# Optimization experiments

Measured on AMD Instinct MI355X. Metric: run time of the kernel, lower is better.

Reference implementation:

```python
import jax, jax.numpy as jnp
import numpy as np

N = 50000      # nodes
E = 800000     # edges
G = 64         # graphs in batch
H = 256        # hidden_channels
CE = 128       # coord embed dim = H//2
OTH = 6        # in_channels - 3
ED = 8         # edge_dim
EE = 128       # edge_embedding_dim
GD = 16        # global_dim
L = 3          # num_layers


def setup_inputs() -> dict:
    key = jax.random.key(0)
    ks = jax.random.split(key, 24)
    s = 0.05
    inp = {
        "x": jax.random.normal(ks[0], (N, 9), jnp.float32),
        "edge_index": jax.random.randint(ks[1], (2, E), 0, N),
        "batch": jnp.sort(jax.random.randint(ks[2], (N,), 0, G)),
        "edge_attr": jax.random.normal(ks[3], (E, ED), jnp.float32),
        "global_x": jax.random.normal(ks[4], (G, GD), jnp.float32),
        # coordinate embedder (Linear 3->128 + relu)
        "coord_W": jax.random.normal(ks[5], (3, CE), jnp.float32) * s,
        "coord_b": jnp.zeros((CE,), jnp.float32),
        # node_mlp (Linear 6->128 + relu)
        "node_W": jax.random.normal(ks[6], (OTH, CE), jnp.float32) * s,
        "node_b": jnp.zeros((CE,), jnp.float32),
        # edge processor (Linear 8->128 + relu) and projection 128->256
        "edge_W": jax.random.normal(ks[7], (ED, EE), jnp.float32) * s,
        "edge_b": jnp.zeros((EE,), jnp.float32),
        "proj_W": jax.random.normal(ks[8], (EE, H), jnp.float32) * s,
        "proj_b": jnp.zeros((H,), jnp.float32),
        # stacked GCN layer weights
        "gcn_W": jax.random.normal(ks[9], (L, H, H), jnp.float32) * s,
        "gcn_b": jnp.zeros((L, H), jnp.float32),
        # attention pooling
        "attn_w": jax.random.normal(ks[10], (H,), jnp.float32) * s,
        "attn_b": jnp.zeros((), jnp.float32),
        # global_mlp: Linear 16->256, relu, Linear 256->256
        "gmlp_W1": jax.random.normal(ks[11], (GD, H), jnp.float32) * s,
        "gmlp_b1": jnp.zeros((H,), jnp.float32),
        "gmlp_W2": jax.random.normal(ks[12], (H, H), jnp.float32) * s,
        "gmlp_b2": jnp.zeros((H,), jnp.float32),
        # fc_out: Linear 512->256, relu, Linear 256->1
        "fc_W1": jax.random.normal(ks[13], (2 * H, H), jnp.float32) * s,
        "fc_b1": jnp.zeros((H,), jnp.float32),
        "fc_W2": jax.random.normal(ks[14], (H, 1), jnp.float32) * s,
        "fc_b2": jnp.zeros((1,), jnp.float32),
    }
    return inp


def _segsum(v, idx, num):
    return jax.ops.segment_sum(v, idx, num_segments=num)


def reference(x, edge_index, batch, edge_attr, global_x,
              coord_W, coord_b, node_W, node_b, edge_W, edge_b,
              proj_W, proj_b, gcn_W, gcn_b, attn_w, attn_b,
              gmlp_W1, gmlp_b1, gmlp_W2, gmlp_b2,
              fc_W1, fc_b1, fc_W2, fc_b2):
    relu = jax.nn.relu
    # --- node embedding: coords + other features ---
    coord_emb = relu(x[:, :3] @ coord_W + coord_b)          # [N, 128]
    other_emb = relu(x[:, 3:] @ node_W + node_b)            # [N, 128]
    x_emb = jnp.concatenate([coord_emb, other_emb], axis=1)  # [N, 256]

    # --- edge embedding, aggregated to target nodes (index_add over col) ---
    edge_emb = relu(edge_attr @ edge_W + edge_b) @ proj_W + proj_b  # [E, 256]
    col0 = edge_index[1]
    node_msg = _segsum(edge_emb, col0, N)                    # [N, 256]

    # --- GCN normalization with self-loops ---
    sl = jnp.arange(N)
    row = jnp.concatenate([edge_index[0], sl])
    col = jnp.concatenate([edge_index[1], sl])
    deg = _segsum(jnp.ones_like(col, jnp.float32), col, N)   # >= 1
    dnorm = jax.lax.rsqrt(deg)
    efac = (dnorm[row] * dnorm[col])[:, None]                # [E+N, 1]

    # --- stacked GCN layers (edge messages re-added each layer, per source) ---
    for i in range(L):
        x_in = x_emb + node_msg
        h = x_in @ gcn_W[i]                                  # [N, 256]
        x_emb = _segsum(h[row] * efac, col, N) + gcn_b[i]
        if i < L - 1:
            x_emb = relu(x_emb)

    # --- attention pooling (per-graph softmax over batch index) ---
    scores = x_emb @ attn_w + attn_b                         # [N]
    m = jax.ops.segment_max(scores, batch, num_segments=G)
    e = jnp.exp(scores - m[batch])
    denom = _segsum(e, batch, G)
    attn = e / denom[batch]
    graph_emb = _segsum(x_emb * attn[:, None], batch, G)     # [G, 256]

    # --- global features + head ---
    g = relu(global_x @ gmlp_W1 + gmlp_b1) @ gmlp_W2 + gmlp_b2
    hcat = jnp.concatenate([graph_emb, g], axis=-1)          # [G, 512]
    out = relu(hcat @ fc_W1 + fc_b1) @ fc_W2 + fc_b2         # [G, 1]
    return out
```

## Files before the change

kernel.cpp:

```cpp
#include <hip/hip_runtime.h>


typedef float f32x4 __attribute__((ext_vector_type(4)));
typedef short s16x8 __attribute__((ext_vector_type(8)));

__device__ __forceinline__ unsigned short f2bf(float f) {
  union { float f; unsigned u; } v{f};
  unsigned r = v.u + 0x7fff + ((v.u >> 16) & 1);
  return (unsigned short)(r >> 16);
}
__device__ __forceinline__ float bf2f(unsigned short s) {
  union { unsigned u; float f; } v{(unsigned)s << 16};
  return v.f;
}
__device__ __forceinline__ float blo(unsigned u) {
  union { unsigned x; float f; } v{u << 16};
  return v.f;
}
__device__ __forceinline__ float bhi(unsigned u) {
  union { unsigned x; float f; } v{u & 0xffff0000u};
  return v.f;
}
__device__ __forceinline__ unsigned pk2(float a, float b) {
  return (unsigned)f2bf(a) | ((unsigned)f2bf(b) << 16);
}

__global__ void node_embed_kernel(const float* __restrict__ x,
                                  const float* __restrict__ coord_W, const float* __restrict__ coord_b,
                                  const float* __restrict__ node_W, const float* __restrict__ node_b,
                                  short* __restrict__ x0, int N) {
  int tid = threadIdx.x;
  int node = blockIdx.x * 8 + (tid >> 5);
  if (node >= N) return;
  int ch0 = (tid & 31) * 8;
  const float* xr = x + (size_t)node * 9;
  float a[8];
  if (ch0 < 128) {
    float4 b0 = *(const float4*)&coord_b[ch0];
    float4 b1 = *(const float4*)&coord_b[ch0 + 4];
    a[0]=b0.x; a[1]=b0.y; a[2]=b0.z; a[3]=b0.w; a[4]=b1.x; a[5]=b1.y; a[6]=b1.z; a[7]=b1.w;
#pragma unroll
    for (int k = 0; k < 3; k++) {
      float xv = xr[k];
      float4 w0 = *(const float4*)&coord_W[k * 128 + ch0];
      float4 w1 = *(const float4*)&coord_W[k * 128 + ch0 + 4];
      a[0] = fmaf(xv, w0.x, a[0]); a[1] = fmaf(xv, w0.y, a[1]);
      a[2] = fmaf(xv, w0.z, a[2]); a[3] = fmaf(xv, w0.w, a[3]);
      a[4] = fmaf(xv, w1.x, a[4]); a[5] = fmaf(xv, w1.y, a[5]);
      a[6] = fmaf(xv, w1.z, a[6]); a[7] = fmaf(xv, w1.w, a[7]);
    }
  } else {
    int c0 = ch0 - 128;
    float4 b0 = *(const float4*)&node_b[c0];
    float4 b1 = *(const float4*)&node_b[c0 + 4];
    a[0]=b0.x; a[1]=b0.y; a[2]=b0.z; a[3]=b0.w; a[4]=b1.x; a[5]=b1.y; a[6]=b1.z; a[7]=b1.w;
#pragma unroll
    for (int k = 0; k < 6; k++) {
      float xv = xr[3 + k];
      float4 w0 = *(const float4*)&node_W[k * 128 + c0];
      float4 w1 = *(const float4*)&node_W[k * 128 + c0 + 4];
      a[0] = fmaf(xv, w0.x, a[0]); a[1] = fmaf(xv, w0.y, a[1]);
      a[2] = fmaf(xv, w0.z, a[2]); a[3] = fmaf(xv, w0.w, a[3]);
      a[4] = fmaf(xv, w1.x, a[4]); a[5] = fmaf(xv, w1.y, a[5]);
      a[6] = fmaf(xv, w1.z, a[6]); a[7] = fmaf(xv, w1.w, a[7]);
    }
  }
  uint4 o;
  o.x = pk2(fmaxf(a[0], 0.f), fmaxf(a[1], 0.f));
  o.y = pk2(fmaxf(a[2], 0.f), fmaxf(a[3], 0.f));
  o.z = pk2(fmaxf(a[4], 0.f), fmaxf(a[5], 0.f));
  o.w = pk2(fmaxf(a[6], 0.f), fmaxf(a[7], 0.f));
  *(uint4*)&x0[(size_t)node * 256 + ch0] = o;
}

__global__ void count_kernel(const int* __restrict__ col, int* __restrict__ cnt, int E) {
  int e = blockIdx.x * 256 + threadIdx.x;
  if (e < E) atomicAdd(&cnt[col[e]], 1);
}

__global__ void breduce_kernel(const int* __restrict__ cnt, int* __restrict__ partials, int N) {
  __shared__ int red[256];
  int t = threadIdx.x;
  int i = blockIdx.x * 256 + t;
  int v = (i < N) ? cnt[i] : 0;
  red[t] = v;
  __syncthreads();
  for (int off = 128; off; off >>= 1) {
    if (t < off) red[t] += red[t + off];
    __syncthreads();
  }
  if (t == 0) partials[blockIdx.x] = red[0];
}

__global__ void scan_partials_kernel(int* __restrict__ partials, int nb) {
  __shared__ int s[1024];
  int t = threadIdx.x;
  for (int i = t; i < nb; i += 256) s[i] = partials[i];
  __syncthreads();
  if (t == 0) {
    int run = 0;
    for (int i = 0; i < nb; i++) { int c = s[i]; s[i] = run; run += c; }
  }
  __syncthreads();
  for (int i = t; i < nb; i += 256) partials[i] = s[i];
}

__global__ void scan_apply_kernel(const int* __restrict__ cnt, const int* __restrict__ partials,
                                  int* __restrict__ rowstart, float* __restrict__ dnorm,
                                  int* __restrict__ cursor, int N) {
  __shared__ int red[256];
  int t = threadIdx.x;
  int i = blockIdx.x * 256 + t;
  int v = (i < N) ? cnt[i] : 0;
  red[t] = v;
  __syncthreads();
  for (int off = 1; off < 256; off <<= 1) {
    int x = (t >= off) ? red[t - off] : 0;
    __syncthreads();
    red[t] += x;
    __syncthreads();
  }
  if (i < N) {
    int ex = red[t] - v + partials[blockIdx.x];
    rowstart[i] = ex;
    dnorm[i] = rsqrtf((float)(v + 1));
    cursor[i] = 0;
    if (i == N - 1) rowstart[N] = ex + v;
  }
}

__global__ void scatter_kernel(const int* __restrict__ row, const int* __restrict__ col,
                               const int* __restrict__ rowstart, int* __restrict__ cursor,
                               const float* __restrict__ dnorm,
                               int2* __restrict__ pk8, int* __restrict__ eids, int E) {
  int e = blockIdx.x * 256 + threadIdx.x;
  if (e >= E) return;
  int c = col[e], r = row[e];
  int p = atomicAdd(&cursor[c], 1);
  int slot = rowstart[c] + p;
  pk8[slot] = make_int2(r, __float_as_int(dnorm[r] * dnorm[c]));
  eids[slot] = e;
}

__global__ void wt_kernel(const float* __restrict__ gcn_W, const float* __restrict__ proj_W,
                          short* __restrict__ gcnWt, short* __restrict__ projWt) {
  int idx = blockIdx.x * 256 + threadIdx.x;
  if (idx < 3 * 65536) {
    int l = idx >> 16, r = idx & 65535, n = r >> 8, k = r & 255;
    gcnWt[idx] = (short)f2bf(gcn_W[l * 65536 + k * 256 + n]);
  } else {
    int j = idx - 3 * 65536;
    int n = j >> 7, k = j & 127;
    projWt[j] = (short)f2bf(proj_W[k * 256 + n]);
  }
}

__global__ void __launch_bounds__(256) edge_msg_kernel(
    const float* __restrict__ edge_attr, const int* __restrict__ eids,
    const int* __restrict__ rowstart,
    const float* __restrict__ edge_W, const float* __restrict__ edge_b,
    unsigned* __restrict__ msg128u, int N) {
  int lane = threadIdx.x & 63;
  int node = blockIdx.x * 4 + (threadIdx.x >> 6);
  if (node >= N) return;
  int ch0 = lane * 2;
  float wa[8], wb[8];
#pragma unroll
  for (int k = 0; k < 8; k++) {
    float2 w = *(const float2*)&edge_W[k * 128 + ch0];
    wa[k] = w.x; wb[k] = w.y;
  }
  float2 bb = *(const float2*)&edge_b[ch0];
  float acc0 = 0.f, acc1 = 0.f;
  int s = rowstart[node], s1 = rowstart[node + 1];
  const float4* ea4 = (const float4*)edge_attr;
  for (; s + 4 <= s1; s += 4) {
    int e0 = eids[s], e1 = eids[s + 1], e2 = eids[s + 2], e3 = eids[s + 3];
    float4 a00 = ea4[(size_t)e0 * 2], a01 = ea4[(size_t)e0 * 2 + 1];
    float4 a10 = ea4[(size_t)e1 * 2], a11 = ea4[(size_t)e1 * 2 + 1];
    float4 a20 = ea4[(size_t)e2 * 2], a21 = ea4[(size_t)e2 * 2 + 1];
    float4 a30 = ea4[(size_t)e3 * 2], a31 = ea4[(size_t)e3 * 2 + 1];
    float t0, t1;
#define EMLP(lo, hi)                                                        \
    t0 = bb.x; t1 = bb.y;                                                   \
    t0 = fmaf(lo.x, wa[0], t0); t1 = fmaf(lo.x, wb[0], t1);                 \
    t0 = fmaf(lo.y, wa[1], t0); t1 = fmaf(lo.y, wb[1], t1);                 \
    t0 = fmaf(lo.z, wa[2], t0); t1 = fmaf(lo.z, wb[2], t1);                 \
    t0 = fmaf(lo.w, wa[3], t0); t1 = fmaf(lo.w, wb[3], t1);                 \
    t0 = fmaf(hi.x, wa[4], t0); t1 = fmaf(hi.x, wb[4], t1);                 \
    t0 = fmaf(hi.y, wa[5], t0); t1 = fmaf(hi.y, wb[5], t1);                 \
    t0 = fmaf(hi.z, wa[6], t0); t1 = fmaf(hi.z, wb[6], t1);                 \
    t0 = fmaf(hi.w, wa[7], t0); t1 = fmaf(hi.w, wb[7], t1);                 \
    acc0 += fmaxf(t0, 0.f); acc1 += fmaxf(t1, 0.f);
    EMLP(a00, a01)
    EMLP(a10, a11)
    EMLP(a20, a21)
    EMLP(a30, a31)
  }
  for (; s < s1; s++) {
    int e = eids[s];
    float4 lo = ea4[(size_t)e * 2], hi = ea4[(size_t)e * 2 + 1];
    float t0, t1;
    EMLP(lo, hi)
  }
#undef EMLP
  msg128u[(size_t)node * 64 + lane] = pk2(acc0, acc1);
}

__global__ void __launch_bounds__(256) proj_gemm_mfma(
    const short* __restrict__ msg128, const short* __restrict__ projWt,
    const float* __restrict__ proj_b, const int* __restrict__ cnt,
    short* __restrict__ node_msg, int N) {
  __shared__ short As[64][136];
  int tid = threadIdx.x;
  int n0 = blockIdx.x * 64;
  for (int i = tid; i < 64 * 32; i += 256) {
    int r = i >> 5, c4 = (i & 31) << 2;
    int n = n0 + r;
    uint2 v = make_uint2(0, 0);
    if (n < N) v = *(const uint2*)&msg128[(size_t)n * 128 + c4];
    *(uint2*)&As[r][c4] = v;
  }
  __syncthreads();
  int wave = tid >> 6, lane = tid & 63;
  int mrow = wave * 16 + (lane & 15);
  int kgrp = (lane >> 4) * 8;
  f32x4 acc[16];
#pragma unroll
  for (int i = 0; i < 16; i++) acc[i] = (f32x4){0.f, 0.f, 0.f, 0.f};
  const short* wbase = projWt + (size_t)(lane & 15) * 128 + kgrp;
#pragma unroll
  for (int kk = 0; kk < 4; kk++) {
    s16x8 a = *(const s16x8*)&As[mrow][kk * 32 + kgrp];
#pragma unroll
    for (int nf = 0; nf < 16; nf++) {
      s16x8 b = *(const s16x8*)&wbase[(size_t)nf * 16 * 128 + kk * 32];
      acc[nf] = __builtin_amdgcn_mfma_f32_16x16x32_bf16(a, b, acc[nf], 0, 0, 0);
    }
  }
  int orow0 = wave * 16 + (lane >> 4) * 4;
  int ocol = lane & 15;
#pragma unroll
  for (int r = 0; r < 4; r++) {
    int n = n0 + orow0 + r;
    if (n < N) {
      float cn = (float)cnt[n];
#pragma unroll
      for (int nf = 0; nf < 16; nf++) {
        int c = nf * 16 + ocol;
        node_msg[(size_t)n * 256 + c] = (short)f2bf(acc[nf][r] + cn * proj_b[c]);
      }
    }
  }
}

__global__ void __launch_bounds__(256) gcn_gemm_add_mfma(
    const short* __restrict__ X, const short* __restrict__ M,
    const short* __restrict__ Wt, short* __restrict__ Hout, int N) {
  __shared__ short As[64][264];
  int tid = threadIdx.x;
  int n0 = blockIdx.x * 64;
  for (int i = tid; i < 64 * 64; i += 256) {
    int r = i >> 6, c4 = (i & 63) << 2;
    int n = n0 + r;
    uint2 o = make_uint2(0, 0);
    if (n < N) {
      uint2 xv = *(const uint2*)&X[(size_t)n * 256 + c4];
      uint2 mv = *(const uint2*)&M[(size_t)n * 256 + c4];
      o.x = pk2(blo(xv.x) + blo(mv.x), bhi(xv.x) + bhi(mv.x));
      o.y = pk2(blo(xv.y) + blo(mv.y), bhi(xv.y) + bhi(mv.y));
    }
    *(uint2*)&As[r][c4] = o;
  }
  __syncthreads();
  int wave = tid >> 6, lane = tid & 63;
  int mrow = wave * 16 + (lane & 15);
  int kgrp = (lane >> 4) * 8;
  f32x4 acc[16];
#pragma unroll
  for (int i = 0; i < 16; i++) acc[i] = (f32x4){0.f, 0.f, 0.f, 0.f};
  const short* wbase = Wt + (size_t)(lane & 15) * 256 + kgrp;
#pragma unroll
  for (int kk = 0; kk < 8; kk++) {
    s16x8 a = *(const s16x8*)&As[mrow][kk * 32 + kgrp];
#pragma unroll
    for (int nf = 0; nf < 16; nf++) {
      s16x8 b = *(const s16x8*)&wbase[(size_t)nf * 16 * 256 + kk * 32];
      acc[nf] = __builtin_amdgcn_mfma_f32_16x16x32_bf16(a, b, acc[nf], 0, 0, 0);
    }
  }
  int orow0 = wave * 16 + (lane >> 4) * 4;
  int ocol = lane & 15;
#pragma unroll
  for (int nf = 0; nf < 16; nf++) {
#pragma unroll
    for (int r = 0; r < 4; r++) {
      int n = n0 + orow0 + r;
      if (n < N) Hout[(size_t)n * 256 + nf * 16 + ocol] = (short)f2bf(acc[nf][r]);
    }
  }
}

__global__ void __launch_bounds__(256) gcn_agg_kernel(
    const short* __restrict__ h, const int2* __restrict__ pk8,
    const int* __restrict__ rowstart, const float* __restrict__ dnorm,
    const float* __restrict__ b, const short* __restrict__ node_msg,
    short* __restrict__ xin, int N) {
  int lane = threadIdx.x & 63;
  int node = blockIdx.x * 4 + (threadIdx.x >> 6);
  if (node >= N) return;
  int ch0 = lane << 2;
  size_t rowb = (size_t)node * 256 + ch0;
  float dn = dnorm[node];
  float wgt = dn * dn;
  uint2 hv = *(const uint2*)&h[rowb];
  float a0 = blo(hv.x) * wgt, a1 = bhi(hv.x) * wgt;
  float a2 = blo(hv.y) * wgt, a3 = bhi(hv.y) * wgt;
  int s = rowstart[node], s1 = rowstart[node + 1];
  for (; s + 4 <= s1; s += 4) {
    int2 p0 = pk8[s], p1 = pk8[s + 1], p2 = pk8[s + 2], p3 = pk8[s + 3];
    float f0 = __int_as_float(p0.y), f1 = __int_as_float(p1.y);
    float f2 = __int_as_float(p2.y), f3 = __int_as_float(p3.y);
    uint2 v0 = *(const uint2*)&h[(size_t)p0.x * 256 + ch0];
    uint2 v1 = *(const uint2*)&h[(size_t)p1.x * 256 + ch0];
    uint2 v2 = *(const uint2*)&h[(size_t)p2.x * 256 + ch0];
    uint2 v3 = *(const uint2*)&h[(size_t)p3.x * 256 + ch0];
    a0 = fmaf(blo(v0.x), f0, a0); a1 = fmaf(bhi(v0.x), f0, a1);
    a2 = fmaf(blo(v0.y), f0, a2); a3 = fmaf(bhi(v0.y), f0, a3);
    a0 = fmaf(blo(v1.x), f1, a0); a1 = fmaf(bhi(v1.x), f1, a1);
    a2 = fmaf(blo(v1.y), f1, a2); a3 = fmaf(bhi(v1.y), f1, a3);
    a0 = fmaf(blo(v2.x), f2, a0); a1 = fmaf(bhi(v2.x), f2, a1);
    a2 = fmaf(blo(v2.y), f2, a2); a3 = fmaf(bhi(v2.y), f2, a3);
    a0 = fmaf(blo(v3.x), f3, a0); a1 = fmaf(bhi(v3.x), f3, a1);
    a2 = fmaf(blo(v3.y), f3, a2); a3 = fmaf(bhi(v3.y), f3, a3);
  }
  for (; s < s1; s++) {
    int2 p = pk8[s];
    float f = __int_as_float(p.y);
    uint2 v = *(const uint2*)&h[(size_t)p.x * 256 + ch0];
    a0 = fmaf(blo(v.x), f, a0); a1 = fmaf(bhi(v.x), f, a1);
    a2 = fmaf(blo(v.y), f, a2); a3 = fmaf(bhi(v.y), f, a3);
  }
  float4 bv = *(const float4*)&b[ch0];
  uint2 mv = *(const uint2*)&node_msg[rowb];
  float y0 = fmaxf(a0 + bv.x, 0.f) + blo(mv.x);
  float y1 = fmaxf(a1 + bv.y, 0.f) + bhi(mv.x);
  float y2 = fmaxf(a2 + bv.z, 0.f) + blo(mv.y);
  float y3 = fmaxf(a3 + bv.w, 0.f) + bhi(mv.y);
  uint2 o;
  o.x = pk2(y0, y1);
  o.y = pk2(y2, y3);
  *(uint2*)&xin[rowb] = o;
}

__global__ void __launch_bounds__(256) gcn_gemm_mfma(
    const short* __restrict__ Xin, const short* __restrict__ Wt,
    short* __restrict__ Hout, int N) {
  __shared__ short As[64][264];
  int tid = threadIdx.x;
  int n0 = blockIdx.x * 64;
  for (int i = tid; i < 64 * 64; i += 256) {
    int r = i >> 6, c4 = (i & 63) << 2;
    int n = n0 + r;
    uint2 v = make_uint2(0, 0);
    if (n < N) v = *(const uint2*)&Xin[(size_t)n * 256 + c4];
    *(uint2*)&As[r][c4] = v;
  }
  __syncthreads();
  int wave = tid >> 6, lane = tid & 63;
  int mrow = wave * 16 + (lane & 15);
  int kgrp = (lane >> 4) * 8;
  f32x4 acc[16];
#pragma unroll
  for (int i = 0; i < 16; i++) acc[i] = (f32x4){0.f, 0.f, 0.f, 0.f};
  const short* wbase = Wt + (size_t)(lane & 15) * 256 + kgrp;
#pragma unroll
  for (int kk = 0; kk < 8; kk++) {
    s16x8 a = *(const s16x8*)&As[mrow][kk * 32 + kgrp];
#pragma unroll
    for (int nf = 0; nf < 16; nf++) {
      s16x8 b = *(const s16x8*)&wbase[(size_t)nf * 16 * 256 + kk * 32];
      acc[nf] = __builtin_amdgcn_mfma_f32_16x16x32_bf16(a, b, acc[nf], 0, 0, 0);
    }
  }
  int orow0 = wave * 16 + (lane >> 4) * 4;
  int ocol = lane & 15;
#pragma unroll
  for (int nf = 0; nf < 16; nf++) {
#pragma unroll
    for (int r = 0; r < 4; r++) {
      int n = n0 + orow0 + r;
      if (n < N) Hout[(size_t)n * 256 + nf * 16 + ocol] = (short)f2bf(acc[nf][r]);
    }
  }
}

__global__ void __launch_bounds__(256) final_agg_kernel(
    const short* __restrict__ h, const int2* __restrict__ pk8,
    const int* __restrict__ rowstart, const float* __restrict__ dnorm,
    const float* __restrict__ b, short* __restrict__ x_emb,
    const float* __restrict__ attn_w, const float* __restrict__ attn_b,
    float* __restrict__ scores, int N) {
  int lane = threadIdx.x & 63;
  int node = blockIdx.x * 4 + (threadIdx.x >> 6);
  if (node >= N) return;
  int ch0 = lane << 2;
  size_t rowb = (size_t)node * 256 + ch0;
  float dn = dnorm[node];
  float wgt = dn * dn;
  uint2 hv = *(const uint2*)&h[rowb];
  float a0 = blo(hv.x) * wgt, a1 = bhi(hv.x) * wgt;
  float a2 = blo(hv.y) * wgt, a3 = bhi(hv.y) * wgt;
  int s = rowstart[node], s1 = rowstart[node + 1];
  for (; s + 4 <= s1; s += 4) {
    int2 p0 = pk8[s], p1 = pk8[s + 1], p2 = pk8[s + 2], p3 = pk8[s + 3];
    float f0 = __int_as_float(p0.y), f1 = __int_as_float(p1.y);
    float f2 = __int_as_float(p2.y), f3 = __int_as_float(p3.y);
    uint2 v0 = *(const uint2*)&h[(size_t)p0.x * 256 + ch0];
    uint2 v1 = *(const uint2*)&h[(size_t)p1.x * 256 + ch0];
    uint2 v2 = *(const uint2*)&h[(size_t)p2.x * 256 + ch0];
    uint2 v3 = *(const uint2*)&h[(size_t)p3.x * 256 + ch0];
    a0 = fmaf(blo(v0.x), f0, a0); a1 = fmaf(bhi(v0.x), f0, a1);
    a2 = fmaf(blo(v0.y), f0, a2); a3 = fmaf(bhi(v0.y), f0, a3);
    a0 = fmaf(blo(v1.x), f1, a0); a1 = fmaf(bhi(v1.x), f1, a1);
    a2 = fmaf(blo(v1.y), f1, a2); a3 = fmaf(bhi(v1.y), f1, a3);
    a0 = fmaf(blo(v2.x), f2, a0); a1 = fmaf(bhi(v2.x), f2, a1);
    a2 = fmaf(blo(v2.y), f2, a2); a3 = fmaf(bhi(v2.y), f2, a3);
    a0 = fmaf(blo(v3.x), f3, a0); a1 = fmaf(bhi(v3.x), f3, a1);
    a2 = fmaf(blo(v3.y), f3, a2); a3 = fmaf(bhi(v3.y), f3, a3);
  }
  for (; s < s1; s++) {
    int2 p = pk8[s];
    float f = __int_as_float(p.y);
    uint2 v = *(const uint2*)&h[(size_t)p.x * 256 + ch0];
    a0 = fmaf(blo(v.x), f, a0); a1 = fmaf(bhi(v.x), f, a1);
    a2 = fmaf(blo(v.y), f, a2); a3 = fmaf(bhi(v.y), f, a3);
  }
  float4 bv = *(const float4*)&b[ch0];
  a0 += bv.x; a1 += bv.y; a2 += bv.z; a3 += bv.w;
  uint2 o;
  o.x = pk2(a0, a1);
  o.y = pk2(a2, a3);
  *(uint2*)&x_emb[rowb] = o;
  float4 aw = *(const float4*)&attn_w[ch0];
  float p = a0 * aw.x + a1 * aw.y + a2 * aw.z + a3 * aw.w;
#pragma unroll
  for (int off = 32; off; off >>= 1) p += __shfl_down(p, off);
  if (lane == 0) scores[node] = p + attn_b[0];
}

__global__ void gse_kernel(const int* __restrict__ batch, int* __restrict__ gs,
                           int* __restrict__ ge, int N) {
  int i = blockIdx.x * 256 + threadIdx.x;
  if (i >= N) return;
  int g = batch[i];
  if (i == 0) gs[g] = 0;
  else {
    int gp = batch[i - 1];
    if (gp != g) { gs[g] = i; ge[gp] = i - 1; }
  }
  if (i == N - 1) ge[g] = N - 1;
}

__global__ void softmax_kernel(const float* __restrict__ scores, const int* __restrict__ gs,
                               const int* __restrict__ ge, float* __restrict__ wnode) {
  int g = blockIdx.x;
  int tid = threadIdx.x;
  __shared__ float red[256];
  int s0 = gs[g], e1 = ge[g];
  if (s0 > e1) return;
  int s1 = e1 + 1;
  float m = -1e30f;
  for (int i = s0 + tid; i < s1; i += 256) m = fmaxf(m, scores[i]);
  red[tid] = m;
  __syncthreads();
  for (int off = 128; off; off >>= 1) {
    if (tid < off) red[tid] = fmaxf(red[tid], red[tid + off]);
    __syncthreads();
  }
  m = red[0];
  __syncthreads();
  float d = 0.f;
  for (int i = s0 + tid; i < s1; i += 256) d += expf(scores[i] - m);
  red[tid] = d;
  __syncthreads();
  for (int off = 128; off; off >>= 1) {
    if (tid < off) red[tid] += red[tid + off];
    __syncthreads();
  }
  float rd = 1.f / red[0];
  for (int i = s0 + tid; i < s1; i += 256) wnode[i] = expf(scores[i] - m) * rd;
}

__global__ void __launch_bounds__(256) pool_sum_kernel(
    const short* __restrict__ x_emb, const float* __restrict__ wnode,
    const int* __restrict__ batch, float* __restrict__ graph_emb, int N) {
  __shared__ int sb[256];
  __shared__ float sw[256];
  int ch = threadIdx.x;
  int i0 = blockIdx.x * 256;
  int lim = min(256, N - i0);
  if (ch < lim) { sb[ch] = batch[i0 + ch]; sw[ch] = wnode[i0 + ch]; }
  __syncthreads();
  int curg = sb[0];
  float acc = 0.f;
  for (int j = 0; j < lim; j++) {
    int g = sb[j];
    if (g != curg) {
      atomicAdd(&graph_emb[(size_t)curg * 256 + ch], acc);
      acc = 0.f;
      curg = g;
    }
    acc = fmaf(bf2f((unsigned short)x_emb[(size_t)(i0 + j) * 256 + ch]), sw[j], acc);
  }
  atomicAdd(&graph_emb[(size_t)curg * 256 + ch], acc);
}

__global__ void head_kernel(const float* __restrict__ global_x, const float* __restrict__ graph_emb,
                            const float* __restrict__ W1, const float* __restrict__ b1,
                            const float* __restrict__ W2, const float* __restrict__ b2,
                            const float* __restrict__ fW1, const float* __restrict__ fb1,
                            const float* __restrict__ fW2, const float* __restrict__ fb2,
                            float* __restrict__ out) {
  int g = blockIdx.x;
  int ch = threadIdx.x;
  __shared__ float t1[256], g2s[256], t3s[256];
  float a = b1[ch];
  const float* gx = global_x + g * 16;
#pragma unroll
  for (int k = 0; k < 16; k++) a = fmaf(gx[k], W1[k * 256 + ch], a);
  t1[ch] = fmaxf(a, 0.f);
  __syncthreads();
  float bb = b2[ch];
  for (int k = 0; k < 256; k++) bb = fmaf(t1[k], W2[k * 256 + ch], bb);
  g2s[ch] = bb;
  __syncthreads();
  float c = fb1[ch];
  const float* ger = graph_emb + (size_t)g * 256;
  for (int k = 0; k < 256; k++) c = fmaf(ger[k], fW1[k * 256 + ch], c);
  for (int k = 0; k < 256; k++) c = fmaf(g2s[k], fW1[(256 + k) * 256 + ch], c);
  t3s[ch] = fmaxf(c, 0.f);
  __syncthreads();
  t1[ch] = t3s[ch] * fW2[ch];
  __syncthreads();
  for (int off = 128; off; off >>= 1) {
    if (ch < off) t1[ch] += t1[ch + off];
    __syncthreads();
  }
  if (ch == 0) out[g] = t1[0] + fb2[0];
}

extern "C" void kernel_launch(void* const* d_in, const int* in_sizes, int n_in,
                              void* d_out, int out_size, void* d_ws, size_t ws_size,
                              hipStream_t stream) {
  const float* x        = (const float*)d_in[0];
  const int*   ei       = (const int*)d_in[1];
  const int*   batch    = (const int*)d_in[2];
  const float* edge_attr= (const float*)d_in[3];
  const float* global_x = (const float*)d_in[4];
  const float* coord_W  = (const float*)d_in[5];
  const float* coord_b  = (const float*)d_in[6];
  const float* node_W   = (const float*)d_in[7];
  const float* node_b   = (const float*)d_in[8];
  const float* edge_W   = (const float*)d_in[9];
  const float* edge_b   = (const float*)d_in[10];
  const float* proj_W   = (const float*)d_in[11];
  const float* proj_b   = (const float*)d_in[12];
  const float* gcn_W    = (const float*)d_in[13];
  const float* gcn_b    = (const float*)d_in[14];
  const float* attn_w   = (const float*)d_in[15];
  const float* attn_b   = (const float*)d_in[16];
  const float* gmlp_W1  = (const float*)d_in[17];
  const float* gmlp_b1  = (const float*)d_in[18];
  const float* gmlp_W2  = (const float*)d_in[19];
  const float* gmlp_b2  = (const float*)d_in[20];
  const float* fc_W1    = (const float*)d_in[21];
  const float* fc_b1    = (const float*)d_in[22];
  const float* fc_W2    = (const float*)d_in[23];
  const float* fc_b2    = (const float*)d_in[24];

  const int N = in_sizes[0] / 9;
  const int E = in_sizes[3] / 8;
  const int G = in_sizes[4] / 16;
  const int NB = (N + 255) / 256;

  char* w = (char*)d_ws;
  auto alloc = [&](size_t bytes) -> char* {
    char* p = w;
    w += (bytes + 255) & ~(size_t)255;
    return p;
  };
  short* x0       = (short*)alloc((size_t)N * 256 * 2);
  short* node_msg = (short*)alloc((size_t)N * 256 * 2);
  short* hA       = (short*)alloc((size_t)N * 256 * 2);
  short* hB       = (short*)alloc((size_t)N * 256 * 2);
  short* xinBuf   = (short*)alloc((size_t)N * 256 * 2);
  short* x_emb    = (short*)alloc((size_t)N * 256 * 2);
  short* msg128   = x_emb;
  int2*  pk8      = (int2*)alloc((size_t)E * 8);
  int*   eids     = (int*)alloc((size_t)E * 4);
  short* gcnWt    = (short*)alloc((size_t)3 * 65536 * 2);
  short* projWt   = (short*)alloc((size_t)256 * 128 * 2);
  int*   cnt      = (int*)alloc((size_t)N * 4);
  int*   rowstart = (int*)alloc((size_t)(N + 1) * 4);
  int*   cursor   = (int*)alloc((size_t)N * 4);
  float* dnorm    = (float*)alloc((size_t)N * 4);
  float* scores   = (float*)alloc((size_t)N * 4);
  float* wnode    = (float*)alloc((size_t)N * 4);
  int*   partials = (int*)alloc((size_t)NB * 4);
  int*   gs       = (int*)alloc((size_t)G * 4);
  int*   ge       = (int*)alloc((size_t)G * 4);
  float* graph_emb= (float*)alloc((size_t)G * 256 * 4);

  hipMemsetAsync(cnt, 0, (size_t)N * 4, stream);
  hipMemsetAsync(gs, 0x7f, (size_t)G * 4, stream);
  hipMemsetAsync(ge, 0xff, (size_t)G * 4, stream);
  hipMemsetAsync(graph_emb, 0, (size_t)G * 256 * 4, stream);

  wt_kernel<<<(3 * 65536 + 256 * 128 + 255) / 256, 256, 0, stream>>>(gcn_W, proj_W, gcnWt, projWt);
  node_embed_kernel<<<(N + 7) / 8, 256, 0, stream>>>(
      x, coord_W, coord_b, node_W, node_b, x0, N);
  count_kernel<<<(E + 255) / 256, 256, 0, stream>>>(ei + E, cnt, E);
  breduce_kernel<<<NB, 256, 0, stream>>>(cnt, partials, N);
  scan_partials_kernel<<<1, 256, 0, stream>>>(partials, NB);
  scan_apply_kernel<<<NB, 256, 0, stream>>>(cnt, partials, rowstart, dnorm, cursor, N);
  scatter_kernel<<<(E + 255) / 256, 256, 0, stream>>>(
      ei, ei + E, rowstart, cursor, dnorm, pk8, eids, E);
  edge_msg_kernel<<<(N + 3) / 4, 256, 0, stream>>>(
      edge_attr, eids, rowstart, edge_W, edge_b, (unsigned*)msg128, N);
  proj_gemm_mfma<<<(N + 63) / 64, 256, 0, stream>>>(
      msg128, projWt, proj_b, cnt, node_msg, N);
  gcn_gemm_add_mfma<<<(N + 63) / 64, 256, 0, stream>>>(
      x0, node_msg, gcnWt, hA, N);
  gcn_agg_kernel<<<(N + 3) / 4, 256, 0, stream>>>(
      hA, pk8, rowstart, dnorm, gcn_b, node_msg, xinBuf, N);
  gcn_gemm_mfma<<<(N + 63) / 64, 256, 0, stream>>>(
      xinBuf, gcnWt + 65536, hB, N);
  gcn_agg_kernel<<<(N + 3) / 4, 256, 0, stream>>>(
      hB, pk8, rowstart, dnorm, gcn_b + 256, node_msg, xinBuf, N);
  gcn_gemm_mfma<<<(N + 63) / 64, 256, 0, stream>>>(
      xinBuf, gcnWt + 2 * 65536, hA, N);
  final_agg_kernel<<<(N + 3) / 4, 256, 0, stream>>>(
      hA, pk8, rowstart, dnorm, gcn_b + 512, x_emb, attn_w, attn_b, scores, N);
  gse_kernel<<<(N + 255) / 256, 256, 0, stream>>>(batch, gs, ge, N);
  softmax_kernel<<<G, 256, 0, stream>>>(scores, gs, ge, wnode);
  pool_sum_kernel<<<NB, 256, 0, stream>>>(x_emb, wnode, batch, graph_emb, N);
  head_kernel<<<G, 256, 0, stream>>>(global_x, graph_emb, gmlp_W1, gmlp_b1, gmlp_W2, gmlp_b2,
                                     fc_W1, fc_b1, fc_W2, fc_b2, (float*)d_out);
}
```

Before: 923.4 us.

## Split GEMM output columns across blocks and stage weight tiles in LDS

The three MFMA GEMM kernels (projection and GCN layers) now use a 2D grid in which each block computes a 64-column slice of the output. The matching 64-row slice of the transposed weights is staged in shared memory instead of being read directly from global memory per MFMA. Each block now needs only 4 accumulators instead of 16, which lowers register pressure and quadruples the block count. In exchange, the A tile is reloaded from global memory four times, and shared memory per block roughly doubles.

```diff
diff --git a/kernel.cpp b/kernel.cpp
--- a/kernel.cpp
+++ b/kernel.cpp
@@ -212,29 +212,32 @@
     const float* __restrict__ proj_b, const int* __restrict__ cnt,
     short* __restrict__ node_msg, int N) {
   __shared__ short As[64][136];
+  __shared__ short Bs[64][136];
   int tid = threadIdx.x;
   int n0 = blockIdx.x * 64;
+  int cb = blockIdx.y * 64;
   for (int i = tid; i < 64 * 32; i += 256) {
     int r = i >> 5, c4 = (i & 31) << 2;
     int n = n0 + r;
     uint2 v = make_uint2(0, 0);
     if (n < N) v = *(const uint2*)&msg128[(size_t)n * 128 + c4];
     *(uint2*)&As[r][c4] = v;
+    *(uint2*)&Bs[r][c4] = *(const uint2*)&projWt[(size_t)(cb + r) * 128 + c4];
   }
   __syncthreads();
   int wave = tid >> 6, lane = tid & 63;
   int mrow = wave * 16 + (lane & 15);
+  int brow = lane & 15;
   int kgrp = (lane >> 4) * 8;
-  f32x4 acc[16];
-#pragma unroll
-  for (int i = 0; i < 16; i++) acc[i] = (f32x4){0.f, 0.f, 0.f, 0.f};
-  const short* wbase = projWt + (size_t)(lane & 15) * 128 + kgrp;
+  f32x4 acc[4];
+#pragma unroll
+  for (int i = 0; i < 4; i++) acc[i] = (f32x4){0.f, 0.f, 0.f, 0.f};
 #pragma unroll
   for (int kk = 0; kk < 4; kk++) {
     s16x8 a = *(const s16x8*)&As[mrow][kk * 32 + kgrp];
 #pragma unroll
-    for (int nf = 0; nf < 16; nf++) {
-      s16x8 b = *(const s16x8*)&wbase[(size_t)nf * 16 * 128 + kk * 32];
+    for (int nf = 0; nf < 4; nf++) {
+      s16x8 b = *(const s16x8*)&Bs[nf * 16 + brow][kk * 32 + kgrp];
       acc[nf] = __builtin_amdgcn_mfma_f32_16x16x32_bf16(a, b, acc[nf], 0, 0, 0);
     }
   }
@@ -246,8 +249,8 @@
     if (n < N) {
       float cn = (float)cnt[n];
 #pragma unroll
-      for (int nf = 0; nf < 16; nf++) {
-        int c = nf * 16 + ocol;
+      for (int nf = 0; nf < 4; nf++) {
+        int c = cb + nf * 16 + ocol;
         node_msg[(size_t)n * 256 + c] = (short)f2bf(acc[nf][r] + cn * proj_b[c]);
       }
     }
@@ -258,8 +261,10 @@
     const short* __restrict__ X, const short* __restrict__ M,
     const short* __restrict__ Wt, short* __restrict__ Hout, int N) {
   __shared__ short As[64][264];
+  __shared__ short Bs[64][264];
   int tid = threadIdx.x;
   int n0 = blockIdx.x * 64;
+  int cb = blockIdx.y * 64;
   for (int i = tid; i < 64 * 64; i += 256) {
     int r = i >> 6, c4 = (i & 63) << 2;
     int n = n0 + r;
@@ -271,32 +276,78 @@
       o.y = pk2(blo(xv.y) + blo(mv.y), bhi(xv.y) + bhi(mv.y));
     }
     *(uint2*)&As[r][c4] = o;
+    *(uint2*)&Bs[r][c4] = *(const uint2*)&Wt[(size_t)(cb + r) * 256 + c4];
   }
   __syncthreads();
   int wave = tid >> 6, lane = tid & 63;
   int mrow = wave * 16 + (lane & 15);
+  int brow = lane & 15;
   int kgrp = (lane >> 4) * 8;
-  f32x4 acc[16];
-#pragma unroll
-  for (int i = 0; i < 16; i++) acc[i] = (f32x4){0.f, 0.f, 0.f, 0.f};
-  const short* wbase = Wt + (size_t)(lane & 15) * 256 + kgrp;
+  f32x4 acc[4];
+#pragma unroll
+  for (int i = 0; i < 4; i++) acc[i] = (f32x4){0.f, 0.f, 0.f, 0.f};
 #pragma unroll
   for (int kk = 0; kk < 8; kk++) {
     s16x8 a = *(const s16x8*)&As[mrow][kk * 32 + kgrp];
 #pragma unroll
-    for (int nf = 0; nf < 16; nf++) {
-      s16x8 b = *(const s16x8*)&wbase[(size_t)nf * 16 * 256 + kk * 32];
+    for (int nf = 0; nf < 4; nf++) {
+      s16x8 b = *(const s16x8*)&Bs[nf * 16 + brow][kk * 32 + kgrp];
       acc[nf] = __builtin_amdgcn_mfma_f32_16x16x32_bf16(a, b, acc[nf], 0, 0, 0);
     }
   }
   int orow0 = wave * 16 + (lane >> 4) * 4;
   int ocol = lane & 15;
 #pragma unroll
-  for (int nf = 0; nf < 16; nf++) {
+  for (int nf = 0; nf < 4; nf++) {
 #pragma unroll
     for (int r = 0; r < 4; r++) {
       int n = n0 + orow0 + r;
-      if (n < N) Hout[(size_t)n * 256 + nf * 16 + ocol] = (short)f2bf(acc[nf][r]);
+      if (n < N) Hout[(size_t)n * 256 + cb + nf * 16 + ocol] = (short)f2bf(acc[nf][r]);
+    }
+  }
+}
+
+__global__ void __launch_bounds__(256) gcn_gemm_mfma(
+    const short* __restrict__ Xin, const short* __restrict__ Wt,
+    short* __restrict__ Hout, int N) {
+  __shared__ short As[64][264];
+  __shared__ short Bs[64][264];
+  int tid = threadIdx.x;
+  int n0 = blockIdx.x * 64;
+  int cb = blockIdx.y * 64;
+  for (int i = tid; i < 64 * 64; i += 256) {
+    int r = i >> 6, c4 = (i & 63) << 2;
+    int n = n0 + r;
+    uint2 v = make_uint2(0, 0);
+    if (n < N) v = *(const uint2*)&Xin[(size_t)n * 256 + c4];
+    *(uint2*)&As[r][c4] = v;
+    *(uint2*)&Bs[r][c4] = *(const uint2*)&Wt[(size_t)(cb + r) * 256 + c4];
+  }
+  __syncthreads();
+  int wave = tid >> 6, lane = tid & 63;
+  int mrow = wave * 16 + (lane & 15);
+  int brow = lane & 15;
+  int kgrp = (lane >> 4) * 8;
+  f32x4 acc[4];
+#pragma unroll
+  for (int i = 0; i < 4; i++) acc[i] = (f32x4){0.f, 0.f, 0.f, 0.f};
+#pragma unroll
+  for (int kk = 0; kk < 8; kk++) {
+    s16x8 a = *(const s16x8*)&As[mrow][kk * 32 + kgrp];
+#pragma unroll
+    for (int nf = 0; nf < 4; nf++) {
+      s16x8 b = *(const s16x8*)&Bs[nf * 16 + brow][kk * 32 + kgrp];
+      acc[nf] = __builtin_amdgcn_mfma_f32_16x16x32_bf16(a, b, acc[nf], 0, 0, 0);
+    }
+  }
+  int orow0 = wave * 16 + (lane >> 4) * 4;
+  int ocol = lane & 15;
+#pragma unroll
+  for (int nf = 0; nf < 4; nf++) {
+#pragma unroll
+    for (int r = 0; r < 4; r++) {
+      int n = n0 + orow0 + r;
+      if (n < N) Hout[(size_t)n * 256 + cb + nf * 16 + ocol] = (short)f2bf(acc[nf][r]);
     }
   }
 }
@@ -351,48 +402,6 @@
   o.x = pk2(y0, y1);
   o.y = pk2(y2, y3);
   *(uint2*)&xin[rowb] = o;
-}
-
-__global__ void __launch_bounds__(256) gcn_gemm_mfma(
-    const short* __restrict__ Xin, const short* __restrict__ Wt,
-    short* __restrict__ Hout, int N) {
-  __shared__ short As[64][264];
-  int tid = threadIdx.x;
-  int n0 = blockIdx.x * 64;
-  for (int i = tid; i < 64 * 64; i += 256) {
-    int r = i >> 6, c4 = (i & 63) << 2;
-    int n = n0 + r;
-    uint2 v = make_uint2(0, 0);
-    if (n < N) v = *(const uint2*)&Xin[(size_t)n * 256 + c4];
-    *(uint2*)&As[r][c4] = v;
-  }
-  __syncthreads();
-  int wave = tid >> 6, lane = tid & 63;
-  int mrow = wave * 16 + (lane & 15);
-  int kgrp = (lane >> 4) * 8;
-  f32x4 acc[16];
-#pragma unroll
-  for (int i = 0; i < 16; i++) acc[i] = (f32x4){0.f, 0.f, 0.f, 0.f};
-  const short* wbase = Wt + (size_t)(lane & 15) * 256 + kgrp;
-#pragma unroll
-  for (int kk = 0; kk < 8; kk++) {
-    s16x8 a = *(const s16x8*)&As[mrow][kk * 32 + kgrp];
-#pragma unroll
-    for (int nf = 0; nf < 16; nf++) {
-      s16x8 b = *(const s16x8*)&wbase[(size_t)nf * 16 * 256 + kk * 32];
-      acc[nf] = __builtin_amdgcn_mfma_f32_16x16x32_bf16(a, b, acc[nf], 0, 0, 0);
-    }
-  }
-  int orow0 = wave * 16 + (lane >> 4) * 4;
-  int ocol = lane & 15;
-#pragma unroll
-  for (int nf = 0; nf < 16; nf++) {
-#pragma unroll
-    for (int r = 0; r < 4; r++) {
-      int n = n0 + orow0 + r;
-      if (n < N) Hout[(size_t)n * 256 + nf * 16 + ocol] = (short)f2bf(acc[nf][r]);
-    }
-  }
 }
 
 __global__ void __launch_bounds__(256) final_agg_kernel(
@@ -583,6 +592,7 @@
   const int E = in_sizes[3] / 8;
   const int G = in_sizes[4] / 16;
   const int NB = (N + 255) / 256;
+  const int NM = (N + 63) / 64;
 
   char* w = (char*)d_ws;
   auto alloc = [&](size_t bytes) -> char* {
@@ -628,17 +638,17 @@
       ei, ei + E, rowstart, cursor, dnorm, pk8, eids, E);
   edge_msg_kernel<<<(N + 3) / 4, 256, 0, stream>>>(
       edge_attr, eids, rowstart, edge_W, edge_b, (unsigned*)msg128, N);
-  proj_gemm_mfma<<<(N + 63) / 64, 256, 0, stream>>>(
+  proj_gemm_mfma<<<dim3(NM, 4), 256, 0, stream>>>(
       msg128, projWt, proj_b, cnt, node_msg, N);
-  gcn_gemm_add_mfma<<<(N + 63) / 64, 256, 0, stream>>>(
+  gcn_gemm_add_mfma<<<dim3(NM, 4), 256, 0, stream>>>(
       x0, node_msg, gcnWt, hA, N);
   gcn_agg_kernel<<<(N + 3) / 4, 256, 0, stream>>>(
       hA, pk8, rowstart, dnorm, gcn_b, node_msg, xinBuf, N);
-  gcn_gemm_mfma<<<(N + 63) / 64, 256, 0, stream>>>(
+  gcn_gemm_mfma<<<dim3(NM, 4), 256, 0, stream>>>(
       xinBuf, gcnWt + 65536, hB, N);
   gcn_agg_kernel<<<(N + 3) / 4, 256, 0, stream>>>(
       hB, pk8, rowstart, dnorm, gcn_b + 256, node_msg, xinBuf, N);
-  gcn_gemm_mfma<<<(N + 63) / 64, 256, 0, stream>>>(
+  gcn_gemm_mfma<<<dim3(NM, 4), 256, 0, stream>>>(
       xinBuf, gcnWt + 2 * 65536, hA, N);
   final_agg_kernel<<<(N + 3) / 4, 256, 0, stream>>>(
       hA, pk8, rowstart, dnorm, gcn_b + 512, x_emb, attn_w, attn_b, scores, N);
```

New measurement: 867.1 us. 1.06x faster.
